# Kernel tuning notes

Hardware: AMD Instinct MI355X
Metric: run time of the kernel (lower is better)

## Reference

```python
import jax, jax.numpy as jnp
import numpy as np

N = 8192       # num nodes == voc_size (action_size)
R = 2          # total_rel
B = 2          # n_basis
D0, D1 = 128, 64  # num_layers = [128, 64]


def setup_inputs() -> dict:
    key = jax.random.key(0)
    k0, k1, k2, k3, k4 = jax.random.split(key, 5)
    adj = jax.random.uniform(k0, (R, N, N), dtype=jnp.float32)  # dense relational adjacency
    basis_weight0 = jax.random.normal(k1, (B, N, D0), dtype=jnp.float32) * (1.0 / np.float32(np.sqrt(N)))
    basis_coeff0 = jax.random.normal(k2, (R, B), dtype=jnp.float32) * 0.5
    basis_weight1 = jax.random.normal(k3, (B, D0, D1), dtype=jnp.float32) * (1.0 / np.float32(np.sqrt(D0)))
    basis_coeff1 = jax.random.normal(k4, (R, B), dtype=jnp.float32) * 0.5
    return {
        "adj": adj,
        "basis_weight0": basis_weight0,
        "basis_coeff0": basis_coeff0,
        "basis_weight1": basis_weight1,
        "basis_coeff1": basis_coeff1,
    }


def reference(adj, basis_weight0, basis_coeff0, basis_weight1, basis_coeff1):
    # Layer 0: inp is None -> tmp = concat(adj_r, axis=1) [N, R*N]; out0 = tmp @ W0_flat.
    # Equivalent fused form: out0 = sum_r adj[r] @ W0[r]  (avoids the [N, R*N] concat).
    W0 = jnp.einsum('rb,bno->rno', basis_coeff0, basis_weight0)   # [R, N, D0]
    out0 = jnp.einsum('rnm,rmo->no', adj, W0)                     # [N, D0]

    # Layer 1: relu then per-relation propagate + relation-wise transform.
    h = jax.nn.relu(out0)                                         # [N, D0]
    W1 = jnp.einsum('rb,bmo->rmo', basis_coeff1, basis_weight1)   # [R, D0, D1]
    msgs = jnp.einsum('rnm,mo->rno', adj, h)                      # [R, N, D0]
    out1 = jnp.einsum('rno,rop->np', msgs, W1)                    # [N, D1]

    # final_rep: concat layer outputs along feature dim, sum over nodes -> [1, D0+D1]
    final_rep = jnp.concatenate([out0, out1], axis=1).sum(axis=0).reshape(1, -1)
    return out1, final_rep
```

## Files before the change

### kernel.cpp

```cpp
#include <hip/hip_runtime.h>

typedef __attribute__((ext_vector_type(4))) float f32x4;
typedef __attribute__((ext_vector_type(8))) short s16x8;

#define ADJ_N 8192

__device__ __forceinline__ unsigned short f2bf(float f) {
  unsigned u = __float_as_uint(f);
  u += 0x7FFFu + ((u >> 16) & 1u);
  return (unsigned short)(u >> 16);
}

__global__ __launch_bounds__(256) void build_B0(
    const float* __restrict__ w0, const float* __restrict__ c0,
    unsigned short* __restrict__ Bsw) {
  const int t = blockIdx.x * 256 + threadIdx.x;
  const int ks = t >> 9;
  const int cg = (t >> 6) & 7;
  const int lane = t & 63;
  const int kb = ks * 32 + ((lane >> 4) << 3);
  const int col = cg * 16 + (lane & 15);
  const int r = kb >> 13;
  const int m = kb & (ADJ_N - 1);
  const float a0 = c0[r * 2 + 0], a1 = c0[r * 2 + 1];
  union { unsigned short v[8]; s16x8 s; } out;
#pragma unroll
  for (int j = 0; j < 8; ++j) {
    const size_t idx = (size_t)(m + j) * 128 + col;
    const float f = a0 * w0[idx] + a1 * w0[(size_t)1048576 + idx];
    out.v[j] = f2bf(f);
  }
  ((s16x8*)Bsw)[t] = out.s;
}

__global__ __launch_bounds__(512) void build_B1(
    const float* __restrict__ p0, const float* __restrict__ w1,
    const float* __restrict__ c1, unsigned short* __restrict__ Bsw1,
    float* __restrict__ frep) {
  __shared__ __align__(16) float hs[32][128];
  __shared__ __align__(16) float w1t[2][64 * 128];
  __shared__ float red[512];
  const int tid = threadIdx.x;
  const int m0 = blockIdx.x * 32;

  float cs = 0.f;
  for (int i = tid; i < 32 * 128; i += 512) {
    const int ml = i >> 7, col = i & 127;
    const size_t base = (size_t)(m0 + ml) * 128 + col;
    float s = 0.f;
#pragma unroll
    for (int sp = 0; sp < 8; ++sp)
      s += __builtin_nontemporal_load(&p0[(size_t)sp * 1048576 + base]);
    cs += s;
    hs[ml][col] = fmaxf(s, 0.f);
  }
  const float ca[2][2] = {{c1[0], c1[1]}, {c1[2], c1[3]}};
  for (int i = tid; i < 2 * 64 * 128; i += 512) {
    const int rr = i >> 13;
    const int p = (i >> 7) & 63;
    const int o = i & 127;
    const float v = ca[rr][0] * w1[(size_t)o * 64 + p] + ca[rr][1] * w1[8192 + (size_t)o * 64 + p];
    const int ch = (o >> 2) ^ (p & 31);
    w1t[rr][p * 128 + ch * 4 + (o & 3)] = v;
  }
  red[tid] = cs;
  __syncthreads();
  if (tid < 128)
    atomicAdd(&frep[tid], red[tid] + red[tid + 128] + red[tid + 256] + red[tid + 384]);

  for (int idx = tid; idx < 4096; idx += 512) {
    const int p = idx & 63;
    const int ml = (idx >> 6) & 31;
    const int rr = idx >> 11;
    float s = 0.f;
#pragma unroll
    for (int ch = 0; ch < 32; ++ch) {
      const f32x4 hv = *(const f32x4*)&hs[ml][ch * 4];
      const f32x4 wv = *(const f32x4*)((const char*)&w1t[rr][0] +
                                       ((size_t)p * 32 + (ch ^ (p & 31))) * 16);
      s += hv[0] * wv[0] + hv[1] * wv[1] + hv[2] * wv[2] + hv[3] * wv[3];
    }
    const int k = rr * ADJ_N + m0 + ml;
    const int ks = k >> 5, kin = k & 31;
    const int lane = ((kin >> 3) << 4) | (p & 15);
    const int j = kin & 7;
    const int cg = p >> 4;
    Bsw1[(((size_t)ks * 4 + cg) * 64 + lane) * 8 + j] = f2bf(s);
  }
}

__global__ __launch_bounds__(256, 4) void gemm1_adj(
    const float* __restrict__ adj, const unsigned short* __restrict__ Bfr,
    float* __restrict__ outp, unsigned short* __restrict__ adjB) {
  constexpr int BN = 128, CGS = 8, BK = 64, KRANGE = 2048, NSTEP = 32;
  __shared__ __align__(16) unsigned short Bsb[2][2 * CGS * 512];

  const int bx = blockIdx.x;
  const int mblk = bx >> 3;
  const int split = bx & 7;
  const int n0 = mblk * 64;
  const int k0 = split * KRANGE;
  const int r = k0 >> 13;
  const int m0k = k0 & (ADJ_N - 1);

  const int tid = threadIdx.x;
  const int w = tid >> 6;
  const int lane = tid & 63;
  const int lhi = lane >> 4, llo = lane & 15;
  const int rowa = n0 + w * 16 + llo;

  const float* __restrict__ adjw =
      adj + ((size_t)r << 26) + (size_t)rowa * ADJ_N + m0k + lhi * 8;
  unsigned short* __restrict__ adjBw =
      adjB + ((size_t)r << 26) + (size_t)rowa * ADJ_N + m0k + lhi * 8;

  f32x4 acc[CGS];
#pragma unroll
  for (int b = 0; b < CGS; ++b) acc[b] = (f32x4){0.f, 0.f, 0.f, 0.f};

  auto loadA = [&](int step, f32x4 (&dst)[4]) {
#pragma unroll
    for (int kc = 0; kc < 2; ++kc)
#pragma unroll
      for (int h = 0; h < 2; ++h)
        dst[kc * 2 + h] = __builtin_nontemporal_load(
            (const f32x4*)(adjw + step * BK + kc * 32 + h * 4));
  };

  auto stageB = [&](int buf, int step) {
    const int ksb = (k0 >> 5) + step * 2;
    const unsigned short* g = Bfr + (size_t)ksb * CGS * 512 + w * (CGS / 2) * 512 + lane * 8;
#pragma unroll
    for (int i = 0; i < CGS / 2; ++i) {
      __builtin_amdgcn_global_load_lds(
          (const __attribute__((address_space(1))) void*)(g + i * 512),
          (__attribute__((address_space(3))) void*)((char*)&Bsb[buf][0] +
                                                    (w * (CGS / 2) + i) * 1024),
          16, 0, 0);
    }
  };

  auto compute = [&](int buf, f32x4 (&cur)[4], int s) {
#pragma unroll
    for (int kc = 0; kc < 2; ++kc) {
      union { unsigned u[4]; s16x8 v; } cv;
      asm("v_cvt_pk_bf16_f32 %0, %1, %2" : "=v"(cv.u[0]) : "v"(cur[kc * 2][0]), "v"(cur[kc * 2][1]));
      asm("v_cvt_pk_bf16_f32 %0, %1, %2" : "=v"(cv.u[1]) : "v"(cur[kc * 2][2]), "v"(cur[kc * 2][3]));
      asm("v_cvt_pk_bf16_f32 %0, %1, %2" : "=v"(cv.u[2]) : "v"(cur[kc * 2 + 1][0]), "v"(cur[kc * 2 + 1][1]));
      asm("v_cvt_pk_bf16_f32 %0, %1, %2" : "=v"(cv.u[3]) : "v"(cur[kc * 2 + 1][2]), "v"(cur[kc * 2 + 1][3]));
      *(s16x8*)(adjBw + s * BK + kc * 32) = cv.v;
#pragma unroll
      for (int fc = 0; fc < CGS; ++fc) {
        const s16x8 b = *(const s16x8*)((const char*)&Bsb[buf][0] +
                                        (((kc * CGS + fc) * 64 + lane) << 4));
        acc[fc] = __builtin_amdgcn_mfma_f32_16x16x32_bf16(cv.v, b, acc[fc], 0, 0, 0);
      }
    }
  };

  f32x4 a0[4], a1[4];
  loadA(0, a0);
  stageB(0, 0);
  __syncthreads();

  for (int s2 = 0; s2 < NSTEP; s2 += 2) {
    stageB(1, s2 + 1);
    loadA(s2 + 1, a1);
    compute(0, a0, s2);
    __syncthreads();
    if (s2 + 2 < NSTEP) {
      stageB(0, s2 + 2);
      loadA(s2 + 2, a0);
    }
    compute(1, a1, s2 + 1);
    __syncthreads();
  }

  float* po = outp + ((size_t)split * ADJ_N + (size_t)n0) * BN;
#pragma unroll
  for (int fc = 0; fc < CGS; ++fc)
#pragma unroll
    for (int q = 0; q < 4; ++q)
      __builtin_nontemporal_store(
          acc[fc][q], &po[(size_t)(w * 16 + lhi * 4 + q) * BN + fc * 16 + llo]);
}

__global__ __launch_bounds__(256, 4) void gemm2_adj(
    const unsigned short* __restrict__ adjB, const unsigned short* __restrict__ Bfr,
    float* __restrict__ outp) {
  constexpr int BN = 64, CGS = 4, BK = 64, KRANGE = 2048, NSTEP = 32;
  __shared__ __align__(16) unsigned short Bsb[2][2 * CGS * 512];

  const int bx = blockIdx.x;
  const int mblk = bx >> 3;
  const int split = bx & 7;
  const int n0 = mblk * 64;
  const int k0 = split * KRANGE;
  const int r = k0 >> 13;
  const int m0k = k0 & (ADJ_N - 1);

  const int tid = threadIdx.x;
  const int w = tid >> 6;
  const int lane = tid & 63;
  const int lhi = lane >> 4, llo = lane & 15;
  const int rowa = n0 + w * 16 + llo;

  const unsigned short* __restrict__ adjw =
      adjB + ((size_t)r << 26) + (size_t)rowa * ADJ_N + m0k + lhi * 8;

  f32x4 acc[CGS];
#pragma unroll
  for (int b = 0; b < CGS; ++b) acc[b] = (f32x4){0.f, 0.f, 0.f, 0.f};

  auto loadA = [&](int step, s16x8 (&dst)[2]) {
    dst[0] = *(const s16x8*)(adjw + step * BK);
    dst[1] = *(const s16x8*)(adjw + step * BK + 32);
  };

  auto stageB = [&](int buf, int step) {
    const int ksb = (k0 >> 5) + step * 2;
    const unsigned short* g = Bfr + (size_t)ksb * CGS * 512 + w * (CGS / 2) * 512 + lane * 8;
#pragma unroll
    for (int i = 0; i < CGS / 2; ++i) {
      __builtin_amdgcn_global_load_lds(
          (const __attribute__((address_space(1))) void*)(g + i * 512),
          (__attribute__((address_space(3))) void*)((char*)&Bsb[buf][0] +
                                                    (w * (CGS / 2) + i) * 1024),
          16, 0, 0);
    }
  };

  auto compute = [&](int buf, s16x8 (&cur)[2]) {
#pragma unroll
    for (int kc = 0; kc < 2; ++kc)
#pragma unroll
      for (int fc = 0; fc < CGS; ++fc) {
        const s16x8 b = *(const s16x8*)((const char*)&Bsb[buf][0] +
                                        (((kc * CGS + fc) * 64 + lane) << 4));
        acc[fc] = __builtin_amdgcn_mfma_f32_16x16x32_bf16(cur[kc], b, acc[fc], 0, 0, 0);
      }
  };

  s16x8 a0[2], a1[2];
  loadA(0, a0);
  stageB(0, 0);
  __syncthreads();

  for (int s2 = 0; s2 < NSTEP; s2 += 2) {
    stageB(1, s2 + 1);
    loadA(s2 + 1, a1);
    compute(0, a0);
    __syncthreads();
    if (s2 + 2 < NSTEP) {
      stageB(0, s2 + 2);
      loadA(s2 + 2, a0);
    }
    compute(1, a1);
    __syncthreads();
  }

  float* po = outp + ((size_t)split * ADJ_N + (size_t)n0) * BN;
#pragma unroll
  for (int fc = 0; fc < CGS; ++fc)
#pragma unroll
    for (int q = 0; q < 4; ++q)
      __builtin_nontemporal_store(
          acc[fc][q], &po[(size_t)(w * 16 + lhi * 4 + q) * BN + fc * 16 + llo]);
}

__global__ __launch_bounds__(256) void reduce_out1(
    const float* __restrict__ p1, float* __restrict__ out1,
    float* __restrict__ frep) {
  __shared__ float red[256];
  const int t = threadIdx.x;
  const int col = t & 63, r0 = t >> 6;
  float cs = 0.f;
  for (int k = 0; k < 8; ++k) {
    const size_t row = (size_t)blockIdx.x * 32 + r0 * 8 + k;
    const size_t idx = row * 64 + col;
    float s = 0.f;
#pragma unroll
    for (int sp = 0; sp < 8; ++sp)
      s += __builtin_nontemporal_load(&p1[(size_t)sp * 524288 + idx]);
    out1[idx] = s;
    cs += s;
  }
  red[t] = cs;
  __syncthreads();
  if (t < 64)
    atomicAdd(&frep[128 + t], red[t] + red[t + 64] + red[t + 128] + red[t + 192]);
}

extern "C" void kernel_launch(void* const* d_in, const int* in_sizes, int n_in,
                              void* d_out, int out_size, void* d_ws, size_t ws_size,
                              hipStream_t stream) {
  const float* adj = (const float*)d_in[0];
  const float* bw0 = (const float*)d_in[1];
  const float* bc0 = (const float*)d_in[2];
  const float* bw1 = (const float*)d_in[3];
  const float* bc1 = (const float*)d_in[4];
  float* out = (float*)d_out;
  float* frep = out + (size_t)8192 * 64;

  char* ws = (char*)d_ws;
  float* p0 = (float*)ws;
  float* p1 = (float*)(ws + (32u << 20));
  unsigned short* B0 = (unsigned short*)(ws + (48u << 20));
  unsigned short* B1 = (unsigned short*)(ws + (52u << 20));
  unsigned short* adjB = (unsigned short*)(ws + (64u << 20));

  hipMemsetAsync(frep, 0, 192 * sizeof(float), stream);

  build_B0<<<1024, 256, 0, stream>>>(bw0, bc0, B0);
  gemm1_adj<<<1024, 256, 0, stream>>>(adj, B0, p0, adjB);
  build_B1<<<256, 512, 0, stream>>>(p0, bw1, bc1, B1, frep);
  gemm2_adj<<<1024, 256, 0, stream>>>(adjB, B1, p1);
  reduce_out1<<<256, 256, 0, stream>>>(p1, out, frep);
}
```

Baseline: 313.2 us.

## Drop bf16 adjacency copy, reread fp32 adj in reverse order, MFMA-based B1 build

gemm1 no longer writes a bf16 copy of the adjacency. gemm2 instead rereads the fp32 adjacency directly, walking its K range in reverse so the recently touched tail may still be in cache. The B1 build is split into a reduce/relu kernel and a small MFMA kernel fed by a precomputed bf16 W1 combination, and the frep memset is folded into a kernel. Nontemporal hints are removed. The trade is dropping the 256MB bf16 write against doubling the fp32 reads in the second GEMM, with more kernel launches.

New measurement: 293.9 us. 1.07x faster.

```diff
diff --git a/kernel.cpp b/kernel.cpp
--- a/kernel.cpp
+++ b/kernel.cpp
@@ -33,65 +33,31 @@
   ((s16x8*)Bsw)[t] = out.s;
 }
 
-__global__ __launch_bounds__(512) void build_B1(
-    const float* __restrict__ p0, const float* __restrict__ w1,
-    const float* __restrict__ c1, unsigned short* __restrict__ Bsw1,
-    float* __restrict__ frep) {
-  __shared__ __align__(16) float hs[32][128];
-  __shared__ __align__(16) float w1t[2][64 * 128];
-  __shared__ float red[512];
-  const int tid = threadIdx.x;
-  const int m0 = blockIdx.x * 32;
-
-  float cs = 0.f;
-  for (int i = tid; i < 32 * 128; i += 512) {
-    const int ml = i >> 7, col = i & 127;
-    const size_t base = (size_t)(m0 + ml) * 128 + col;
-    float s = 0.f;
-#pragma unroll
-    for (int sp = 0; sp < 8; ++sp)
-      s += __builtin_nontemporal_load(&p0[(size_t)sp * 1048576 + base]);
-    cs += s;
-    hs[ml][col] = fmaxf(s, 0.f);
-  }
-  const float ca[2][2] = {{c1[0], c1[1]}, {c1[2], c1[3]}};
-  for (int i = tid; i < 2 * 64 * 128; i += 512) {
-    const int rr = i >> 13;
-    const int p = (i >> 7) & 63;
-    const int o = i & 127;
-    const float v = ca[rr][0] * w1[(size_t)o * 64 + p] + ca[rr][1] * w1[8192 + (size_t)o * 64 + p];
-    const int ch = (o >> 2) ^ (p & 31);
-    w1t[rr][p * 128 + ch * 4 + (o & 3)] = v;
-  }
-  red[tid] = cs;
-  __syncthreads();
-  if (tid < 128)
-    atomicAdd(&frep[tid], red[tid] + red[tid + 128] + red[tid + 256] + red[tid + 384]);
-
-  for (int idx = tid; idx < 4096; idx += 512) {
-    const int p = idx & 63;
-    const int ml = (idx >> 6) & 31;
-    const int rr = idx >> 11;
-    float s = 0.f;
-#pragma unroll
-    for (int ch = 0; ch < 32; ++ch) {
-      const f32x4 hv = *(const f32x4*)&hs[ml][ch * 4];
-      const f32x4 wv = *(const f32x4*)((const char*)&w1t[rr][0] +
-                                       ((size_t)p * 32 + (ch ^ (p & 31))) * 16);
-      s += hv[0] * wv[0] + hv[1] * wv[1] + hv[2] * wv[2] + hv[3] * wv[3];
-    }
-    const int k = rr * ADJ_N + m0 + ml;
-    const int ks = k >> 5, kin = k & 31;
-    const int lane = ((kin >> 3) << 4) | (p & 15);
-    const int j = kin & 7;
-    const int cg = p >> 4;
-    Bsw1[(((size_t)ks * 4 + cg) * 64 + lane) * 8 + j] = f2bf(s);
-  }
+__global__ __launch_bounds__(256) void build_W1c(
+    const float* __restrict__ w1, const float* __restrict__ c1,
+    unsigned short* __restrict__ W1c, float* __restrict__ frep) {
+  const int t = blockIdx.x * 256 + threadIdx.x;
+  if (t < 192) frep[t] = 0.f;
+  if (t >= 2048) return;
+  const int f = t >> 6;
+  const int lane = t & 63;
+  const int r = f >> 4;
+  const int ks2 = (f >> 2) & 3;
+  const int cg = f & 3;
+  const float a0 = c1[r * 2 + 0], a1 = c1[r * 2 + 1];
+  union { unsigned short v[8]; s16x8 s; } out;
+#pragma unroll
+  for (int j = 0; j < 8; ++j) {
+    const int o = ks2 * 32 + ((lane >> 4) << 3) + j;
+    const int p = cg * 16 + (lane & 15);
+    out.v[j] = f2bf(a0 * w1[(size_t)o * 64 + p] + a1 * w1[8192 + (size_t)o * 64 + p]);
+  }
+  ((s16x8*)W1c)[t] = out.s;
 }
 
 __global__ __launch_bounds__(256, 4) void gemm1_adj(
     const float* __restrict__ adj, const unsigned short* __restrict__ Bfr,
-    float* __restrict__ outp, unsigned short* __restrict__ adjB) {
+    float* __restrict__ outp) {
   constexpr int BN = 128, CGS = 8, BK = 64, KRANGE = 2048, NSTEP = 32;
   __shared__ __align__(16) unsigned short Bsb[2][2 * CGS * 512];
 
@@ -111,8 +77,6 @@
 
   const float* __restrict__ adjw =
       adj + ((size_t)r << 26) + (size_t)rowa * ADJ_N + m0k + lhi * 8;
-  unsigned short* __restrict__ adjBw =
-      adjB + ((size_t)r << 26) + (size_t)rowa * ADJ_N + m0k + lhi * 8;
 
   f32x4 acc[CGS];
 #pragma unroll
@@ -123,8 +87,7 @@
     for (int kc = 0; kc < 2; ++kc)
 #pragma unroll
       for (int h = 0; h < 2; ++h)
-        dst[kc * 2 + h] = __builtin_nontemporal_load(
-            (const f32x4*)(adjw + step * BK + kc * 32 + h * 4));
+        dst[kc * 2 + h] = *(const f32x4*)(adjw + step * BK + kc * 32 + h * 4);
   };
 
   auto stageB = [&](int buf, int step) {
@@ -140,7 +103,7 @@
     }
   };
 
-  auto compute = [&](int buf, f32x4 (&cur)[4], int s) {
+  auto compute = [&](int buf, f32x4 (&cur)[4]) {
 #pragma unroll
     for (int kc = 0; kc < 2; ++kc) {
       union { unsigned u[4]; s16x8 v; } cv;
@@ -148,7 +111,6 @@
       asm("v_cvt_pk_bf16_f32 %0, %1, %2" : "=v"(cv.u[1]) : "v"(cur[kc * 2][2]), "v"(cur[kc * 2][3]));
       asm("v_cvt_pk_bf16_f32 %0, %1, %2" : "=v"(cv.u[2]) : "v"(cur[kc * 2 + 1][0]), "v"(cur[kc * 2 + 1][1]));
       asm("v_cvt_pk_bf16_f32 %0, %1, %2" : "=v"(cv.u[3]) : "v"(cur[kc * 2 + 1][2]), "v"(cur[kc * 2 + 1][3]));
-      *(s16x8*)(adjBw + s * BK + kc * 32) = cv.v;
 #pragma unroll
       for (int fc = 0; fc < CGS; ++fc) {
         const s16x8 b = *(const s16x8*)((const char*)&Bsb[buf][0] +
@@ -159,89 +121,6 @@
   };
 
   f32x4 a0[4], a1[4];
-  loadA(0, a0);
-  stageB(0, 0);
-  __syncthreads();
-
-  for (int s2 = 0; s2 < NSTEP; s2 += 2) {
-    stageB(1, s2 + 1);
-    loadA(s2 + 1, a1);
-    compute(0, a0, s2);
-    __syncthreads();
-    if (s2 + 2 < NSTEP) {
-      stageB(0, s2 + 2);
-      loadA(s2 + 2, a0);
-    }
-    compute(1, a1, s2 + 1);
-    __syncthreads();
-  }
-
-  float* po = outp + ((size_t)split * ADJ_N + (size_t)n0) * BN;
-#pragma unroll
-  for (int fc = 0; fc < CGS; ++fc)
-#pragma unroll
-    for (int q = 0; q < 4; ++q)
-      __builtin_nontemporal_store(
-          acc[fc][q], &po[(size_t)(w * 16 + lhi * 4 + q) * BN + fc * 16 + llo]);
-}
-
-__global__ __launch_bounds__(256, 4) void gemm2_adj(
-    const unsigned short* __restrict__ adjB, const unsigned short* __restrict__ Bfr,
-    float* __restrict__ outp) {
-  constexpr int BN = 64, CGS = 4, BK = 64, KRANGE = 2048, NSTEP = 32;
-  __shared__ __align__(16) unsigned short Bsb[2][2 * CGS * 512];
-
-  const int bx = blockIdx.x;
-  const int mblk = bx >> 3;
-  const int split = bx & 7;
-  const int n0 = mblk * 64;
-  const int k0 = split * KRANGE;
-  const int r = k0 >> 13;
-  const int m0k = k0 & (ADJ_N - 1);
-
-  const int tid = threadIdx.x;
-  const int w = tid >> 6;
-  const int lane = tid & 63;
-  const int lhi = lane >> 4, llo = lane & 15;
-  const int rowa = n0 + w * 16 + llo;
-
-  const unsigned short* __restrict__ adjw =
-      adjB + ((size_t)r << 26) + (size_t)rowa * ADJ_N + m0k + lhi * 8;
-
-  f32x4 acc[CGS];
-#pragma unroll
-  for (int b = 0; b < CGS; ++b) acc[b] = (f32x4){0.f, 0.f, 0.f, 0.f};
-
-  auto loadA = [&](int step, s16x8 (&dst)[2]) {
-    dst[0] = *(const s16x8*)(adjw + step * BK);
-    dst[1] = *(const s16x8*)(adjw + step * BK + 32);
-  };
-
-  auto stageB = [&](int buf, int step) {
-    const int ksb = (k0 >> 5) + step * 2;
-    const unsigned short* g = Bfr + (size_t)ksb * CGS * 512 + w * (CGS / 2) * 512 + lane * 8;
-#pragma unroll
-    for (int i = 0; i < CGS / 2; ++i) {
-      __builtin_amdgcn_global_load_lds(
-          (const __attribute__((address_space(1))) void*)(g + i * 512),
-          (__attribute__((address_space(3))) void*)((char*)&Bsb[buf][0] +
-                                                    (w * (CGS / 2) + i) * 1024),
-          16, 0, 0);
-    }
-  };
-
-  auto compute = [&](int buf, s16x8 (&cur)[2]) {
-#pragma unroll
-    for (int kc = 0; kc < 2; ++kc)
-#pragma unroll
-      for (int fc = 0; fc < CGS; ++fc) {
-        const s16x8 b = *(const s16x8*)((const char*)&Bsb[buf][0] +
-                                        (((kc * CGS + fc) * 64 + lane) << 4));
-        acc[fc] = __builtin_amdgcn_mfma_f32_16x16x32_bf16(cur[kc], b, acc[fc], 0, 0, 0);
-      }
-  };
-
-  s16x8 a0[2], a1[2];
   loadA(0, a0);
   stageB(0, 0);
   __syncthreads();
@@ -264,8 +143,202 @@
   for (int fc = 0; fc < CGS; ++fc)
 #pragma unroll
     for (int q = 0; q < 4; ++q)
-      __builtin_nontemporal_store(
-          acc[fc][q], &po[(size_t)(w * 16 + lhi * 4 + q) * BN + fc * 16 + llo]);
+      po[(size_t)(w * 16 + lhi * 4 + q) * BN + fc * 16 + llo] = acc[fc][q];
+}
+
+__global__ __launch_bounds__(256) void reduce_h(
+    const float* __restrict__ p0, float* __restrict__ h,
+    float* __restrict__ frep) {
+  __shared__ float red[256];
+  const int t = threadIdx.x;
+  const int col = t & 127, rg = t >> 7;
+  const int n0 = blockIdx.x * 8;
+  float cs = 0.f;
+#pragma unroll
+  for (int rr = 0; rr < 4; ++rr) {
+    const size_t idx = (size_t)(n0 + rg * 4 + rr) * 128 + col;
+    float s = 0.f;
+#pragma unroll
+    for (int sp = 0; sp < 8; ++sp) s += p0[(size_t)sp * 1048576 + idx];
+    cs += s;
+    h[idx] = fmaxf(s, 0.f);
+  }
+  red[t] = cs;
+  __syncthreads();
+  if (t < 128) atomicAdd(&frep[t], red[t] + red[t + 128]);
+}
+
+__global__ __launch_bounds__(128) void build_B1_mfma(
+    const float* __restrict__ h, const unsigned short* __restrict__ W1c,
+    unsigned short* __restrict__ Bsw1) {
+  __shared__ __align__(16) float hs[32][132];
+  __shared__ __align__(16) unsigned short wfr[16384];
+  __shared__ __align__(16) float T[2][16 * 68];
+  const int tid = threadIdx.x;
+  const int m0 = blockIdx.x * 32;
+
+#pragma unroll
+  for (int i = 0; i < 16; ++i) {
+    __builtin_amdgcn_global_load_lds(
+        (const __attribute__((address_space(1))) void*)(W1c + (size_t)(i * 128 + tid) * 8),
+        (__attribute__((address_space(3))) void*)&wfr[(i * 128 + tid) * 8],
+        16, 0, 0);
+  }
+  const f32x4* hg = (const f32x4*)(h + (size_t)m0 * 128);
+#pragma unroll
+  for (int i = 0; i < 8; ++i) {
+    const int v = i * 128 + tid;
+    const f32x4 val = hg[v];
+    *(f32x4*)&hs[v >> 5][(v & 31) * 4] = val;
+  }
+  __syncthreads();
+
+  const int w = tid >> 6;
+  const int lane = tid & 63;
+  const int hi = lane >> 4, llo = lane & 15;
+  const int row = w * 16 + llo;
+
+  f32x4 acc[2][4];
+#pragma unroll
+  for (int r = 0; r < 2; ++r)
+#pragma unroll
+    for (int cg = 0; cg < 4; ++cg) acc[r][cg] = (f32x4){0.f, 0.f, 0.f, 0.f};
+
+#pragma unroll
+  for (int ks2 = 0; ks2 < 4; ++ks2) {
+    const f32x4 lo = *(const f32x4*)&hs[row][ks2 * 32 + hi * 8];
+    const f32x4 hi4 = *(const f32x4*)&hs[row][ks2 * 32 + hi * 8 + 4];
+    union { unsigned u[4]; s16x8 v; } cv;
+    asm("v_cvt_pk_bf16_f32 %0, %1, %2" : "=v"(cv.u[0]) : "v"(lo[0]), "v"(lo[1]));
+    asm("v_cvt_pk_bf16_f32 %0, %1, %2" : "=v"(cv.u[1]) : "v"(lo[2]), "v"(lo[3]));
+    asm("v_cvt_pk_bf16_f32 %0, %1, %2" : "=v"(cv.u[2]) : "v"(hi4[0]), "v"(hi4[1]));
+    asm("v_cvt_pk_bf16_f32 %0, %1, %2" : "=v"(cv.u[3]) : "v"(hi4[2]), "v"(hi4[3]));
+#pragma unroll
+    for (int r = 0; r < 2; ++r)
+#pragma unroll
+      for (int cg = 0; cg < 4; ++cg) {
+        const s16x8 b = *(const s16x8*)&wfr[((r * 16 + ks2 * 4 + cg) * 64 + lane) * 8];
+        acc[r][cg] = __builtin_amdgcn_mfma_f32_16x16x32_bf16(cv.v, b, acc[r][cg], 0, 0, 0);
+      }
+  }
+
+  float* Tw = &T[w][0];
+#pragma unroll
+  for (int r = 0; r < 2; ++r) {
+#pragma unroll
+    for (int cg = 0; cg < 4; ++cg)
+#pragma unroll
+      for (int q = 0; q < 4; ++q)
+        Tw[(hi * 4 + q) * 68 + cg * 16 + llo] = acc[r][cg][q];
+    __builtin_amdgcn_s_waitcnt(0);
+    if ((hi >> 1) == w) {
+      const int mloc0 = 8 * hi - w * 16;
+      const int ks = (r * ADJ_N + m0) >> 5;
+#pragma unroll
+      for (int cg = 0; cg < 4; ++cg) {
+        union { unsigned u[4]; s16x8 v; } pk;
+#pragma unroll
+        for (int jj = 0; jj < 4; ++jj) {
+          const float f0 = Tw[(mloc0 + 2 * jj) * 68 + cg * 16 + llo];
+          const float f1 = Tw[(mloc0 + 2 * jj + 1) * 68 + cg * 16 + llo];
+          asm("v_cvt_pk_bf16_f32 %0, %1, %2" : "=v"(pk.u[jj]) : "v"(f0), "v"(f1));
+        }
+        *(s16x8*)&Bsw1[((size_t)(ks * 4 + cg) * 64 + lane) * 8] = pk.v;
+      }
+    }
+    __builtin_amdgcn_s_waitcnt(0);
+  }
+}
+
+__global__ __launch_bounds__(256, 4) void gemm2_adj(
+    const float* __restrict__ adj, const unsigned short* __restrict__ Bfr,
+    float* __restrict__ outp) {
+  constexpr int BN = 64, CGS = 4, BK = 64, KRANGE = 2048, NSTEP = 32;
+  __shared__ __align__(16) unsigned short Bsb[2][2 * CGS * 512];
+
+  const int bx = blockIdx.x;
+  const int mblk = bx >> 3;
+  const int split = bx & 7;
+  const int n0 = mblk * 64;
+  const int k0 = split * KRANGE;
+  const int r = k0 >> 13;
+  const int m0k = k0 & (ADJ_N - 1);
+
+  const int tid = threadIdx.x;
+  const int w = tid >> 6;
+  const int lane = tid & 63;
+  const int lhi = lane >> 4, llo = lane & 15;
+  const int rowa = n0 + w * 16 + llo;
+
+  const float* __restrict__ adjw =
+      adj + ((size_t)r << 26) + (size_t)rowa * ADJ_N + m0k + lhi * 8;
+
+  f32x4 acc[CGS];
+#pragma unroll
+  for (int b = 0; b < CGS; ++b) acc[b] = (f32x4){0.f, 0.f, 0.f, 0.f};
+
+  auto loadA = [&](int step, f32x4 (&dst)[4]) {
+#pragma unroll
+    for (int kc = 0; kc < 2; ++kc)
+#pragma unroll
+      for (int h = 0; h < 2; ++h)
+        dst[kc * 2 + h] = *(const f32x4*)(adjw + step * BK + kc * 32 + h * 4);
+  };
+
+  auto stageB = [&](int buf, int step) {
+    const int ksb = (k0 >> 5) + step * 2;
+    const unsigned short* g = Bfr + (size_t)ksb * CGS * 512 + w * (CGS / 2) * 512 + lane * 8;
+#pragma unroll
+    for (int i = 0; i < CGS / 2; ++i) {
+      __builtin_amdgcn_global_load_lds(
+          (const __attribute__((address_space(1))) void*)(g + i * 512),
+          (__attribute__((address_space(3))) void*)((char*)&Bsb[buf][0] +
+                                                    (w * (CGS / 2) + i) * 1024),
+          16, 0, 0);
+    }
+  };
+
+  auto compute = [&](int buf, f32x4 (&cur)[4]) {
+#pragma unroll
+    for (int kc = 0; kc < 2; ++kc) {
+      union { unsigned u[4]; s16x8 v; } cv;
+      asm("v_cvt_pk_bf16_f32 %0, %1, %2" : "=v"(cv.u[0]) : "v"(cur[kc * 2][0]), "v"(cur[kc * 2][1]));
+      asm("v_cvt_pk_bf16_f32 %0, %1, %2" : "=v"(cv.u[1]) : "v"(cur[kc * 2][2]), "v"(cur[kc * 2][3]));
+      asm("v_cvt_pk_bf16_f32 %0, %1, %2" : "=v"(cv.u[2]) : "v"(cur[kc * 2 + 1][0]), "v"(cur[kc * 2 + 1][1]));
+      asm("v_cvt_pk_bf16_f32 %0, %1, %2" : "=v"(cv.u[3]) : "v"(cur[kc * 2 + 1][2]), "v"(cur[kc * 2 + 1][3]));
+#pragma unroll
+      for (int fc = 0; fc < CGS; ++fc) {
+        const s16x8 b = *(const s16x8*)((const char*)&Bsb[buf][0] +
+                                        (((kc * CGS + fc) * 64 + lane) << 4));
+        acc[fc] = __builtin_amdgcn_mfma_f32_16x16x32_bf16(cv.v, b, acc[fc], 0, 0, 0);
+      }
+    }
+  };
+
+  f32x4 a0[4], a1[4];
+  loadA(NSTEP - 1, a0);
+  stageB(0, NSTEP - 1);
+  __syncthreads();
+
+  for (int s2 = 0; s2 < NSTEP; s2 += 2) {
+    stageB(1, NSTEP - 2 - s2);
+    loadA(NSTEP - 2 - s2, a1);
+    compute(0, a0);
+    __syncthreads();
+    if (s2 + 2 < NSTEP) {
+      stageB(0, NSTEP - 3 - s2);
+      loadA(NSTEP - 3 - s2, a0);
+    }
+    compute(1, a1);
+    __syncthreads();
+  }
+
+  float* po = outp + ((size_t)split * ADJ_N + (size_t)n0) * BN;
+#pragma unroll
+  for (int fc = 0; fc < CGS; ++fc)
+#pragma unroll
+    for (int q = 0; q < 4; ++q)
+      po[(size_t)(w * 16 + lhi * 4 + q) * BN + fc * 16 + llo] = acc[fc][q];
 }
 
 __global__ __launch_bounds__(256) void reduce_out1(
@@ -273,15 +346,15 @@
     float* __restrict__ frep) {
   __shared__ float red[256];
   const int t = threadIdx.x;
-  const int col = t & 63, r0 = t >> 6;
+  const int col = t & 63, rl = t >> 6;
+  const int n0 = blockIdx.x * 8;
   float cs = 0.f;
-  for (int k = 0; k < 8; ++k) {
-    const size_t row = (size_t)blockIdx.x * 32 + r0 * 8 + k;
-    const size_t idx = row * 64 + col;
+#pragma unroll
+  for (int rr = 0; rr < 2; ++rr) {
+    const size_t idx = (size_t)(n0 + rl * 2 + rr) * 64 + col;
     float s = 0.f;
 #pragma unroll
-    for (int sp = 0; sp < 8; ++sp)
-      s += __builtin_nontemporal_load(&p1[(size_t)sp * 524288 + idx]);
+    for (int sp = 0; sp < 8; ++sp) s += p1[(size_t)sp * 524288 + idx];
     out1[idx] = s;
     cs += s;
   }
@@ -307,13 +380,14 @@
   float* p1 = (float*)(ws + (32u << 20));
   unsigned short* B0 = (unsigned short*)(ws + (48u << 20));
   unsigned short* B1 = (unsigned short*)(ws + (52u << 20));
-  unsigned short* adjB = (unsigned short*)(ws + (64u << 20));
-
-  hipMemsetAsync(frep, 0, 192 * sizeof(float), stream);
-
+  float* h = (float*)(ws + (56u << 20));
+  unsigned short* W1c = (unsigned short*)(ws + (60u << 20));
+
+  build_W1c<<<8, 256, 0, stream>>>(bw1, bc1, W1c, frep);
   build_B0<<<1024, 256, 0, stream>>>(bw0, bc0, B0);
-  gemm1_adj<<<1024, 256, 0, stream>>>(adj, B0, p0, adjB);
-  build_B1<<<256, 512, 0, stream>>>(p0, bw1, bc1, B1, frep);
-  gemm2_adj<<<1024, 256, 0, stream>>>(adjB, B1, p1);
-  reduce_out1<<<256, 256, 0, stream>>>(p1, out, frep);
-}
+  gemm1_adj<<<1024, 256, 0, stream>>>(adj, B0, p0);
+  reduce_h<<<1024, 256, 0, stream>>>(p0, h, frep);
+  build_B1_mfma<<<256, 128, 0, stream>>>(h, W1c, B1);
+  gemm2_adj<<<1024, 256, 0, stream>>>(adj, B1, p1);
+  reduce_out1<<<1024, 256, 0, stream>>>(p1, out, frep);
+}
```
